# Optimization experiments

Hardware: AMD Instinct MI355X
Metric: run time of the kernel (lower is better)

## Reference

```python
import jax, jax.numpy as jnp
import numpy as np

B, S, D = 4, 2048, 1024
H = 16
HD = D // H  # head_dim = key_dim = value_dim = 64


def setup_inputs() -> dict:
    key = jax.random.key(0)
    ks = jax.random.split(key, 4)
    scale = (2.0 / (D + D)) ** 0.5  # xavier_normal for square weight
    return {
        "hidden_states": jax.random.normal(ks[0], (B, S, D), dtype=jnp.float32),
        "Wq": jax.random.normal(ks[1], (D, D), dtype=jnp.float32) * scale,
        "bq": jnp.zeros((D,), dtype=jnp.float32),
        "Wk": jax.random.normal(ks[2], (D, D), dtype=jnp.float32) * scale,
        "bk": jnp.zeros((D,), dtype=jnp.float32),
        "Wv": jax.random.normal(ks[3], (D, D), dtype=jnp.float32) * scale,
        "bv": jnp.zeros((D,), dtype=jnp.float32),
    }


def _split_heads(x):
    # [B, S, H*HD] -> [B, H, S, HD]
    b, s, _ = x.shape
    return x.reshape(b, s, H, HD).transpose(0, 2, 1, 3)


def reference(hidden_states, Wq, bq, Wk, bk, Wv, bv):
    # Linear projections (torch Linear: x @ W.T + b)
    q = _split_heads(hidden_states @ Wq.T + bq)  # [B,H,S,HD]
    k = _split_heads(hidden_states @ Wk.T + bk)
    v = _split_heads(hidden_states @ Wv.T + bv)
    scores = jnp.einsum("bhqd,bhkd->bhqk", q, k) / jnp.sqrt(jnp.float32(HD))
    probs = jax.nn.softmax(scores, axis=-1)
    out = jnp.einsum("bhqk,bhkd->bhqd", probs, v)  # [B,H,S,HD]
    # merge heads -> [B, S, H*HD]
    return out.transpose(0, 2, 1, 3).reshape(B, S, H * HD)
```

## Files before the change

### kernel.cpp

```cpp
#include <hip/hip_runtime.h>
#include <math.h>

#define SB 4
#define SS 2048
#define SD 1024
#define SH 16
#define SHD 64
#define SM (SB * SS)

using f32x4 = __attribute__((ext_vector_type(4))) float;
using h8    = __attribute__((ext_vector_type(8))) _Float16;
using h4    = __attribute__((ext_vector_type(4))) _Float16;
using fp16x2 = __fp16 __attribute__((ext_vector_type(2)));
using fp16x4 = __fp16 __attribute__((ext_vector_type(4)));
using u32x4 = __attribute__((ext_vector_type(4))) unsigned int;

__device__ __forceinline__ unsigned short f2h(float x) {
  _Float16 h = (_Float16)x;
  return __builtin_bit_cast(unsigned short, h);
}

__device__ __forceinline__ void gld_lds16(const unsigned short* g, unsigned short* l) {
  __builtin_amdgcn_global_load_lds(
      (const __attribute__((address_space(1))) unsigned int*)g,
      (__attribute__((address_space(3))) unsigned int*)l, 16, 0, 0);
}

__global__ __launch_bounds__(256) void cvt4h(const float* __restrict__ in,
                                             unsigned short* __restrict__ out, int n4) {
  int i = blockIdx.x * 256 + threadIdx.x;
  if (i >= n4) return;
  float4 v = ((const float4*)in)[i];
  unsigned long long r = (unsigned long long)f2h(v.x)
                       | ((unsigned long long)f2h(v.y) << 16)
                       | ((unsigned long long)f2h(v.z) << 32)
                       | ((unsigned long long)f2h(v.w) << 48);
  ((unsigned long long*)out)[i] = r;
}

__global__ __launch_bounds__(256) void cvt3w(const float* __restrict__ w0, const float* __restrict__ w1,
                                             const float* __restrict__ w2,
                                             unsigned short* __restrict__ o0, unsigned short* __restrict__ o1,
                                             unsigned short* __restrict__ o2) {
  const int z = blockIdx.y;
  const float* in = (z == 0) ? w0 : (z == 1) ? w1 : w2;
  unsigned short* out = (z == 0) ? o0 : (z == 1) ? o1 : o2;
  int i = blockIdx.x * 256 + threadIdx.x;
  float4 v = ((const float4*)in)[i];
  unsigned long long r = (unsigned long long)f2h(v.x)
                       | ((unsigned long long)f2h(v.y) << 16)
                       | ((unsigned long long)f2h(v.z) << 32)
                       | ((unsigned long long)f2h(v.w) << 48);
  ((unsigned long long*)out)[i] = r;
}

__global__ __launch_bounds__(256) void gemm_qkv(
    const unsigned short* __restrict__ Xh,
    const unsigned short* __restrict__ Wqh, const unsigned short* __restrict__ Wkh,
    const unsigned short* __restrict__ Wvh,
    const float* __restrict__ bq, const float* __restrict__ bk, const float* __restrict__ bv,
    unsigned short* __restrict__ Qh, unsigned short* __restrict__ Kh,
    unsigned short* __restrict__ Vt) {
  __shared__ unsigned short lA[128 * 64];
  __shared__ unsigned short lB[128 * 64];
  const int L = blockIdx.x;
  const int xcd = L & 7, rr = L >> 3;
  const int mloc = rr & 7, widx = rr >> 3;
  const int tNi = widx & 7, z = widx >> 3;
  const int tM = (xcd * 8 + mloc) * 128, tN = tNi * 128;

  const unsigned short* W = (z == 0) ? Wqh : (z == 1) ? Wkh : Wvh;
  const float* bias = (z == 0) ? bq : (z == 1) ? bk : bv;

  const int tid = threadIdx.x;
  const int wave = tid >> 6, lane = tid & 63;
  const int quad = lane >> 4, l16 = lane & 15;
  const int wr = (wave >> 1) * 64, wc = (wave & 1) * 64;

  f32x4 acc[4][4] = {};

  const int rB = tid >> 3;
  const int colOff = (((tid & 7) ^ (rB & 7))) * 8;
  const unsigned short* gA[4];
  const unsigned short* gB[4];
#pragma unroll
  for (int i = 0; i < 4; ++i) {
    gA[i] = Xh + (size_t)(tM + i * 32 + rB) * SD + colOff;
    gB[i] = W  + (size_t)(tN + i * 32 + rB) * SD + colOff;
  }
  unsigned short* dA[4];
  unsigned short* dB[4];
#pragma unroll
  for (int i = 0; i < 4; ++i) {
    dA[i] = lA + (i * 256 + wave * 64) * 8;
    dB[i] = lB + (i * 256 + wave * 64) * 8;
  }
  const int swl = l16 & 7;

  if (z == 2) {
    for (int k0 = 0; k0 < SD; k0 += 64) {
      __syncthreads();
#pragma unroll
      for (int i = 0; i < 4; ++i) gld_lds16(gA[i] + k0, dA[i]);
#pragma unroll
      for (int i = 0; i < 4; ++i) gld_lds16(gB[i] + k0, dB[i]);
      __syncthreads();
#pragma unroll
      for (int ks = 0; ks < 2; ++ks) {
        h8 af[4], bf[4];
#pragma unroll
        for (int mi = 0; mi < 4; ++mi)
          af[mi] = *(const h8*)(lA + (wr + mi * 16 + l16) * 64 + (((ks * 4 + quad) ^ swl) * 8));
#pragma unroll
        for (int ni = 0; ni < 4; ++ni)
          bf[ni] = *(const h8*)(lB + (wc + ni * 16 + l16) * 64 + (((ks * 4 + quad) ^ swl) * 8));
#pragma unroll
        for (int mi = 0; mi < 4; ++mi)
#pragma unroll
          for (int ni = 0; ni < 4; ++ni)
            acc[mi][ni] = __builtin_amdgcn_mfma_f32_16x16x32_f16(af[mi], bf[ni], acc[mi][ni], 0, 0, 0);
      }
    }
#pragma unroll
    for (int ni = 0; ni < 4; ++ni) {
      const int gn = tN + wc + ni * 16 + l16;
      const float bb = bias[gn];
#pragma unroll
      for (int mi = 0; mi < 4; ++mi) {
        const int gm = tM + wr + mi * 16 + quad * 4;
        const int vb = gm >> 11, vs = gm & 2047;
        unsigned long long wv = 0;
#pragma unroll
        for (int r = 0; r < 4; ++r)
          wv |= (unsigned long long)f2h(acc[mi][ni][r] + bb) << (16 * r);
        *(unsigned long long*)(Vt + (size_t)(vb * 1024 + gn) * SS + vs) = wv;
      }
    }
  } else {
    for (int k0 = 0; k0 < SD; k0 += 64) {
      __syncthreads();
#pragma unroll
      for (int i = 0; i < 4; ++i) gld_lds16(gA[i] + k0, dA[i]);
#pragma unroll
      for (int i = 0; i < 4; ++i) gld_lds16(gB[i] + k0, dB[i]);
      __syncthreads();
#pragma unroll
      for (int ks = 0; ks < 2; ++ks) {
        h8 af[4], bf[4];
#pragma unroll
        for (int mi = 0; mi < 4; ++mi)
          af[mi] = *(const h8*)(lA + (wr + mi * 16 + l16) * 64 + (((ks * 4 + quad) ^ swl) * 8));
#pragma unroll
        for (int ni = 0; ni < 4; ++ni)
          bf[ni] = *(const h8*)(lB + (wc + ni * 16 + l16) * 64 + (((ks * 4 + quad) ^ swl) * 8));
#pragma unroll
        for (int mi = 0; mi < 4; ++mi)
#pragma unroll
          for (int ni = 0; ni < 4; ++ni)
            acc[mi][ni] = __builtin_amdgcn_mfma_f32_16x16x32_f16(bf[ni], af[mi], acc[mi][ni], 0, 0, 0);
      }
    }
    const float sc = (z == 0) ? 0.18033688011112042f : 1.0f;
    unsigned short* C = (z == 0) ? Qh : Kh;
#pragma unroll
    for (int mi = 0; mi < 4; ++mi) {
      const int gm = tM + wr + mi * 16 + l16;
#pragma unroll
      for (int ni = 0; ni < 4; ++ni) {
        const int gnb = tN + wc + ni * 16 + quad * 4;
        const float4 bb4 = *(const float4*)(bias + gnb);
        unsigned long long wv;
        wv  = (unsigned long long)f2h((acc[mi][ni][0] + bb4.x) * sc);
        wv |= (unsigned long long)f2h((acc[mi][ni][1] + bb4.y) * sc) << 16;
        wv |= (unsigned long long)f2h((acc[mi][ni][2] + bb4.z) * sc) << 32;
        wv |= (unsigned long long)f2h((acc[mi][ni][3] + bb4.w) * sc) << 48;
        *(unsigned long long*)(C + (size_t)gm * SD + gnb) = wv;
      }
    }
  }
}

__global__ __launch_bounds__(256, 4) void attn(const unsigned short* __restrict__ Qh,
                                               const unsigned short* __restrict__ Kh,
                                               const unsigned short* __restrict__ Vt,
                                               float* __restrict__ out) {
  __shared__ unsigned short lK[2][64 * 64];
  __shared__ unsigned short lV[2][64 * 64];
  const int tid = threadIdx.x;
  const int wave = tid >> 6, lane = tid & 63;
  const int quad = lane >> 4, l16 = lane & 15;
  const int bid = blockIdx.x;
  const int bh = bid & 63, qt = bid >> 6;
  const int b = bh >> 4, h = bh & 15;
  const int qs = qt * 128 + wave * 16;

  const unsigned short* qp0 = Qh + ((size_t)(b * SS + qs + l16)) * SD + h * 64 + quad * 8;
  h8 aq[2][2];
#pragma unroll
  for (int x = 0; x < 2; ++x) {
    aq[x][0] = *(const h8*)(qp0 + (size_t)(x * 64) * SD);
    aq[x][1] = *(const h8*)(qp0 + (size_t)(x * 64) * SD + 32);
  }

  const int row0 = tid >> 3, cs0 = (tid & 7) ^ (row0 & 7);
  const int row1 = row0 + 32, cs1 = (tid & 7) ^ (row1 & 7);
  const unsigned short* kS0 = Kh + ((size_t)(b * SS + row0)) * SD + h * 64 + cs0 * 8;
  const unsigned short* kS1 = Kh + ((size_t)(b * SS + row1)) * SD + h * 64 + cs1 * 8;
  const unsigned short* vS0 = Vt + ((size_t)(bh * 64 + row0)) * SS + cs0 * 8;
  const unsigned short* vS1 = Vt + ((size_t)(bh * 64 + row1)) * SS + cs1 * 8;
  unsigned short* dK0 = &lK[0][wave * 512];
  unsigned short* dK1 = &lK[0][2048 + wave * 512];
  unsigned short* dV0 = &lV[0][wave * 512];
  unsigned short* dV1 = &lV[0][2048 + wave * 512];

  f32x4 ov[2][4] = {};
  float lacc[2] = {0.f, 0.f};
  const int swl = l16 & 7;
  const int ko0 = (quad ^ swl) * 8, ko1 = ((4 + quad) ^ swl) * 8;

  gld_lds16(kS0, dK0); gld_lds16(kS1, dK1);
  gld_lds16(vS0, dV0); gld_lds16(vS1, dV1);
  kS0 += 64 * SD; kS1 += 64 * SD; vS0 += 64; vS1 += 64;

  for (int kt = 0; kt < 32; ++kt) {
    const int buf = kt & 1;
    __syncthreads();
    if (kt < 31) {
      const int o = (buf ^ 1) * 64 * 64;
      gld_lds16(kS0, dK0 + o); gld_lds16(kS1, dK1 + o);
      gld_lds16(vS0, dV0 + o); gld_lds16(vS1, dV1 + o);
      kS0 += 64 * SD; kS1 += 64 * SD; vS0 += 64; vS1 += 64;
    }
    const unsigned short* Kt = lK[buf];
    const unsigned short* Vl = lV[buf];

    f32x4 s[2][4];
    __builtin_amdgcn_s_setprio(1);
#pragma unroll
    for (int nt = 0; nt < 4; ++nt) {
      const unsigned short* kr = Kt + (nt * 16 + l16) * 64;
      h8 kf0 = *(const h8*)(kr + ko0);
      h8 kf1 = *(const h8*)(kr + ko1);
#pragma unroll
      for (int x = 0; x < 2; ++x) {
        f32x4 z = {};
        z = __builtin_amdgcn_mfma_f32_16x16x32_f16(kf0, aq[x][0], z, 0, 0, 0);
        s[x][nt] = __builtin_amdgcn_mfma_f32_16x16x32_f16(kf1, aq[x][1], z, 0, 0, 0);
      }
    }
    __builtin_amdgcn_s_setprio(0);

    h8 pb[2][2];
#pragma unroll
    for (int x = 0; x < 2; ++x) {
      unsigned ul[4], uh[4];
      float la = 0.f;
#pragma unroll
      for (int g = 0; g < 4; ++g) {
        float p0 = __builtin_amdgcn_exp2f(s[x][g][0]);
        float p1 = __builtin_amdgcn_exp2f(s[x][g][1]);
        float p2 = __builtin_amdgcn_exp2f(s[x][g][2]);
        float p3 = __builtin_amdgcn_exp2f(s[x][g][3]);
        la += (p0 + p1) + (p2 + p3);
        ul[g] = __builtin_bit_cast(unsigned, __builtin_amdgcn_cvt_pkrtz(p0, p1));
        uh[g] = __builtin_bit_cast(unsigned, __builtin_amdgcn_cvt_pkrtz(p2, p3));
      }
      lacc[x] += la;
      auto sl0 = __builtin_amdgcn_permlane32_swap(ul[0], ul[1], false, false);
      auto tl0 = __builtin_amdgcn_permlane16_swap(sl0[0], sl0[1], false, false);
      auto sh0 = __builtin_amdgcn_permlane32_swap(uh[0], uh[1], false, false);
      auto th0 = __builtin_amdgcn_permlane16_swap(sh0[0], sh0[1], false, false);
      u32x4 w0 = {tl0[0], th0[0], tl0[1], th0[1]};
      pb[x][0] = __builtin_bit_cast(h8, w0);
      auto sl1 = __builtin_amdgcn_permlane32_swap(ul[2], ul[3], false, false);
      auto tl1 = __builtin_amdgcn_permlane16_swap(sl1[0], sl1[1], false, false);
      auto sh1 = __builtin_amdgcn_permlane32_swap(uh[2], uh[3], false, false);
      auto th1 = __builtin_amdgcn_permlane16_swap(sh1[0], sh1[1], false, false);
      u32x4 w1 = {tl1[0], th1[0], tl1[1], th1[1]};
      pb[x][1] = __builtin_bit_cast(h8, w1);
    }

    __builtin_amdgcn_s_setprio(1);
#pragma unroll
    for (int f = 0; f < 4; ++f) {
      const unsigned short* vr = Vl + (f * 16 + l16) * 64;
      h8 v0 = *(const h8*)(vr + ko0);
      h8 v1 = *(const h8*)(vr + ko1);
#pragma unroll
      for (int x = 0; x < 2; ++x) {
        ov[x][f] = __builtin_amdgcn_mfma_f32_16x16x32_f16(v0, pb[x][0], ov[x][f], 0, 0, 0);
        ov[x][f] = __builtin_amdgcn_mfma_f32_16x16x32_f16(v1, pb[x][1], ov[x][f], 0, 0, 0);
      }
    }
    __builtin_amdgcn_s_setprio(0);
  }

#pragma unroll
  for (int x = 0; x < 2; ++x) {
    float lt = lacc[x];
    lt += __shfl_xor(lt, 16);
    lt += __shfl_xor(lt, 32);
    const float inv = 1.0f / lt;
    float* orow = out + ((size_t)(b * SS + qs + x * 64 + l16)) * SD + h * 64 + quad * 4;
#pragma unroll
    for (int f = 0; f < 4; ++f) {
      float4 w;
      w.x = ov[x][f][0] * inv; w.y = ov[x][f][1] * inv;
      w.z = ov[x][f][2] * inv; w.w = ov[x][f][3] * inv;
      *(float4*)(orow + f * 16) = w;
    }
  }
}

extern "C" void kernel_launch(void* const* d_in, const int* in_sizes, int n_in,
                              void* d_out, int out_size, void* d_ws, size_t ws_size,
                              hipStream_t stream) {
  const float* hs = (const float*)d_in[0];
  const float* Wq = (const float*)d_in[1];
  const float* bq = (const float*)d_in[2];
  const float* Wk = (const float*)d_in[3];
  const float* bk = (const float*)d_in[4];
  const float* Wv = (const float*)d_in[5];
  const float* bv = (const float*)d_in[6];
  float* out = (float*)d_out;

  char* ws = (char*)d_ws;
  unsigned short* Xh  = (unsigned short*)(ws);
  unsigned short* Wqh = (unsigned short*)(ws + 16777216);
  unsigned short* Wkh = (unsigned short*)(ws + 16777216 + 2097152);
  unsigned short* Wvh = (unsigned short*)(ws + 16777216 + 2 * 2097152);
  unsigned short* Qh  = (unsigned short*)(ws + 16777216 + 3 * 2097152);
  unsigned short* Kh  = Qh + (size_t)SM * SD;
  unsigned short* Vt  = Kh + (size_t)SM * SD;

  cvt4h<<<dim3(8192), dim3(256), 0, stream>>>(hs, Xh, SM * SD / 4);
  cvt3w<<<dim3(1024, 3), dim3(256), 0, stream>>>(Wq, Wk, Wv, Wqh, Wkh, Wvh);
  gemm_qkv<<<dim3(1536), dim3(256), 0, stream>>>(
      Xh, Wqh, Wkh, Wvh, bq, bk, bv, Qh, Kh, Vt);
  attn<<<dim3(SB * SH * (SS / 128)), dim3(256), 0, stream>>>(Qh, Kh, Vt, out);
}
```

Measured before the change: 242.7 us.

## Merge conversion kernels and triple-buffer attention with 512-thread blocks

The two fp32-to-fp16 conversion kernels become a single launch. The attention kernel grows to 8 waves per block covering 256 query rows, so each K/V tile is loaded once and shared by twice as many queries, with each thread issuing one K and one V load. The double-buffered loop becomes a triple-buffered pipeline that waits with explicit vmcnt and a raw s_barrier, which lets loads run two tiles ahead. The trade-offs are more LDS per block, fewer blocks in the grid, and fragile hand-written waitcnt synchronisation.

```diff
diff --git a/kernel.cpp b/kernel.cpp
--- a/kernel.cpp
+++ b/kernel.cpp
@@ -26,32 +26,28 @@
       (__attribute__((address_space(3))) unsigned int*)l, 16, 0, 0);
 }
 
-__global__ __launch_bounds__(256) void cvt4h(const float* __restrict__ in,
-                                             unsigned short* __restrict__ out, int n4) {
-  int i = blockIdx.x * 256 + threadIdx.x;
-  if (i >= n4) return;
+__global__ __launch_bounds__(256) void cvt_all(const float* __restrict__ hs,
+    const float* __restrict__ w0, const float* __restrict__ w1, const float* __restrict__ w2,
+    unsigned short* __restrict__ xo, unsigned short* __restrict__ o0,
+    unsigned short* __restrict__ o1, unsigned short* __restrict__ o2) {
+  const int bid = blockIdx.x;
+  const float* in;
+  unsigned short* out;
+  int i;
+  if (bid < 8192) {
+    in = hs; out = xo; i = bid * 256 + threadIdx.x;
+  } else {
+    const int r = bid - 8192, z = r >> 10;
+    in = (z == 0) ? w0 : (z == 1) ? w1 : w2;
+    out = (z == 0) ? o0 : (z == 1) ? o1 : o2;
+    i = (r & 1023) * 256 + threadIdx.x;
+  }
   float4 v = ((const float4*)in)[i];
-  unsigned long long r = (unsigned long long)f2h(v.x)
-                       | ((unsigned long long)f2h(v.y) << 16)
-                       | ((unsigned long long)f2h(v.z) << 32)
-                       | ((unsigned long long)f2h(v.w) << 48);
-  ((unsigned long long*)out)[i] = r;
-}
-
-__global__ __launch_bounds__(256) void cvt3w(const float* __restrict__ w0, const float* __restrict__ w1,
-                                             const float* __restrict__ w2,
-                                             unsigned short* __restrict__ o0, unsigned short* __restrict__ o1,
-                                             unsigned short* __restrict__ o2) {
-  const int z = blockIdx.y;
-  const float* in = (z == 0) ? w0 : (z == 1) ? w1 : w2;
-  unsigned short* out = (z == 0) ? o0 : (z == 1) ? o1 : o2;
-  int i = blockIdx.x * 256 + threadIdx.x;
-  float4 v = ((const float4*)in)[i];
-  unsigned long long r = (unsigned long long)f2h(v.x)
-                       | ((unsigned long long)f2h(v.y) << 16)
-                       | ((unsigned long long)f2h(v.z) << 32)
-                       | ((unsigned long long)f2h(v.w) << 48);
-  ((unsigned long long*)out)[i] = r;
+  unsigned long long rr = (unsigned long long)f2h(v.x)
+                        | ((unsigned long long)f2h(v.y) << 16)
+                        | ((unsigned long long)f2h(v.z) << 32)
+                        | ((unsigned long long)f2h(v.w) << 48);
+  ((unsigned long long*)out)[i] = rr;
 }
 
 __global__ __launch_bounds__(256) void gemm_qkv(
@@ -180,120 +176,132 @@
   }
 }
 
-__global__ __launch_bounds__(256, 4) void attn(const unsigned short* __restrict__ Qh,
+__global__ __launch_bounds__(512, 4) void attn(const unsigned short* __restrict__ Qh,
                                                const unsigned short* __restrict__ Kh,
                                                const unsigned short* __restrict__ Vt,
                                                float* __restrict__ out) {
-  __shared__ unsigned short lK[2][64 * 64];
-  __shared__ unsigned short lV[2][64 * 64];
+  __shared__ unsigned short lK[3][64 * 64];
+  __shared__ unsigned short lV[3][64 * 64];
   const int tid = threadIdx.x;
   const int wave = tid >> 6, lane = tid & 63;
   const int quad = lane >> 4, l16 = lane & 15;
   const int bid = blockIdx.x;
   const int bh = bid & 63, qt = bid >> 6;
   const int b = bh >> 4, h = bh & 15;
-  const int qs = qt * 128 + wave * 16;
+  const int qs = qt * 256 + wave * 16;
 
   const unsigned short* qp0 = Qh + ((size_t)(b * SS + qs + l16)) * SD + h * 64 + quad * 8;
   h8 aq[2][2];
 #pragma unroll
   for (int x = 0; x < 2; ++x) {
-    aq[x][0] = *(const h8*)(qp0 + (size_t)(x * 64) * SD);
-    aq[x][1] = *(const h8*)(qp0 + (size_t)(x * 64) * SD + 32);
+    aq[x][0] = *(const h8*)(qp0 + (size_t)(x * 128) * SD);
+    aq[x][1] = *(const h8*)(qp0 + (size_t)(x * 128) * SD + 32);
   }
 
   const int row0 = tid >> 3, cs0 = (tid & 7) ^ (row0 & 7);
-  const int row1 = row0 + 32, cs1 = (tid & 7) ^ (row1 & 7);
   const unsigned short* kS0 = Kh + ((size_t)(b * SS + row0)) * SD + h * 64 + cs0 * 8;
-  const unsigned short* kS1 = Kh + ((size_t)(b * SS + row1)) * SD + h * 64 + cs1 * 8;
   const unsigned short* vS0 = Vt + ((size_t)(bh * 64 + row0)) * SS + cs0 * 8;
-  const unsigned short* vS1 = Vt + ((size_t)(bh * 64 + row1)) * SS + cs1 * 8;
   unsigned short* dK0 = &lK[0][wave * 512];
-  unsigned short* dK1 = &lK[0][2048 + wave * 512];
   unsigned short* dV0 = &lV[0][wave * 512];
-  unsigned short* dV1 = &lV[0][2048 + wave * 512];
 
   f32x4 ov[2][4] = {};
   float lacc[2] = {0.f, 0.f};
   const int swl = l16 & 7;
   const int ko0 = (quad ^ swl) * 8, ko1 = ((4 + quad) ^ swl) * 8;
 
-  gld_lds16(kS0, dK0); gld_lds16(kS1, dK1);
-  gld_lds16(vS0, dV0); gld_lds16(vS1, dV1);
-  kS0 += 64 * SD; kS1 += 64 * SD; vS0 += 64; vS1 += 64;
-
-  for (int kt = 0; kt < 32; ++kt) {
-    const int buf = kt & 1;
-    __syncthreads();
-    if (kt < 31) {
-      const int o = (buf ^ 1) * 64 * 64;
-      gld_lds16(kS0, dK0 + o); gld_lds16(kS1, dK1 + o);
-      gld_lds16(vS0, dV0 + o); gld_lds16(vS1, dV1 + o);
-      kS0 += 64 * SD; kS1 += 64 * SD; vS0 += 64; vS1 += 64;
-    }
-    const unsigned short* Kt = lK[buf];
-    const unsigned short* Vl = lV[buf];
-
-    f32x4 s[2][4];
-    __builtin_amdgcn_s_setprio(1);
-#pragma unroll
-    for (int nt = 0; nt < 4; ++nt) {
-      const unsigned short* kr = Kt + (nt * 16 + l16) * 64;
-      h8 kf0 = *(const h8*)(kr + ko0);
-      h8 kf1 = *(const h8*)(kr + ko1);
-#pragma unroll
-      for (int x = 0; x < 2; ++x) {
-        f32x4 z = {};
-        z = __builtin_amdgcn_mfma_f32_16x16x32_f16(kf0, aq[x][0], z, 0, 0, 0);
-        s[x][nt] = __builtin_amdgcn_mfma_f32_16x16x32_f16(kf1, aq[x][1], z, 0, 0, 0);
-      }
-    }
-    __builtin_amdgcn_s_setprio(0);
-
-    h8 pb[2][2];
-#pragma unroll
-    for (int x = 0; x < 2; ++x) {
-      unsigned ul[4], uh[4];
-      float la = 0.f;
-#pragma unroll
-      for (int g = 0; g < 4; ++g) {
-        float p0 = __builtin_amdgcn_exp2f(s[x][g][0]);
-        float p1 = __builtin_amdgcn_exp2f(s[x][g][1]);
-        float p2 = __builtin_amdgcn_exp2f(s[x][g][2]);
-        float p3 = __builtin_amdgcn_exp2f(s[x][g][3]);
-        la += (p0 + p1) + (p2 + p3);
-        ul[g] = __builtin_bit_cast(unsigned, __builtin_amdgcn_cvt_pkrtz(p0, p1));
-        uh[g] = __builtin_bit_cast(unsigned, __builtin_amdgcn_cvt_pkrtz(p2, p3));
-      }
-      lacc[x] += la;
-      auto sl0 = __builtin_amdgcn_permlane32_swap(ul[0], ul[1], false, false);
-      auto tl0 = __builtin_amdgcn_permlane16_swap(sl0[0], sl0[1], false, false);
-      auto sh0 = __builtin_amdgcn_permlane32_swap(uh[0], uh[1], false, false);
-      auto th0 = __builtin_amdgcn_permlane16_swap(sh0[0], sh0[1], false, false);
-      u32x4 w0 = {tl0[0], th0[0], tl0[1], th0[1]};
-      pb[x][0] = __builtin_bit_cast(h8, w0);
-      auto sl1 = __builtin_amdgcn_permlane32_swap(ul[2], ul[3], false, false);
-      auto tl1 = __builtin_amdgcn_permlane16_swap(sl1[0], sl1[1], false, false);
-      auto sh1 = __builtin_amdgcn_permlane32_swap(uh[2], uh[3], false, false);
-      auto th1 = __builtin_amdgcn_permlane16_swap(sh1[0], sh1[1], false, false);
-      u32x4 w1 = {tl1[0], th1[0], tl1[1], th1[1]};
-      pb[x][1] = __builtin_bit_cast(h8, w1);
-    }
-
-    __builtin_amdgcn_s_setprio(1);
-#pragma unroll
-    for (int f = 0; f < 4; ++f) {
-      const unsigned short* vr = Vl + (f * 16 + l16) * 64;
-      h8 v0 = *(const h8*)(vr + ko0);
-      h8 v1 = *(const h8*)(vr + ko1);
-#pragma unroll
-      for (int x = 0; x < 2; ++x) {
-        ov[x][f] = __builtin_amdgcn_mfma_f32_16x16x32_f16(v0, pb[x][0], ov[x][f], 0, 0, 0);
-        ov[x][f] = __builtin_amdgcn_mfma_f32_16x16x32_f16(v1, pb[x][1], ov[x][f], 0, 0, 0);
-      }
-    }
-    __builtin_amdgcn_s_setprio(0);
-  }
+#define STAGE(BUF) do { \
+    gld_lds16(kS0, dK0 + (BUF) * 4096); \
+    gld_lds16(vS0, dV0 + (BUF) * 4096); \
+    kS0 += 64 * SD; vS0 += 64; \
+  } while (0)
+
+#define COMPUTE(BUF) do { \
+    const unsigned short* Kt = lK[BUF]; \
+    const unsigned short* Vl = lV[BUF]; \
+    f32x4 s[2][4]; \
+    __builtin_amdgcn_s_setprio(1); \
+    _Pragma("unroll") \
+    for (int nt = 0; nt < 4; ++nt) { \
+      const unsigned short* kr = Kt + (nt * 16 + l16) * 64; \
+      h8 kf0 = *(const h8*)(kr + ko0); \
+      h8 kf1 = *(const h8*)(kr + ko1); \
+      _Pragma("unroll") \
+      for (int x = 0; x < 2; ++x) { \
+        f32x4 z = {}; \
+        z = __builtin_amdgcn_mfma_f32_16x16x32_f16(kf0, aq[x][0], z, 0, 0, 0); \
+        s[x][nt] = __builtin_amdgcn_mfma_f32_16x16x32_f16(kf1, aq[x][1], z, 0, 0, 0); \
+      } \
+    } \
+    __builtin_amdgcn_s_setprio(0); \
+    h8 pb[2][2]; \
+    _Pragma("unroll") \
+    for (int x = 0; x < 2; ++x) { \
+      unsigned ul[4], uh[4]; \
+      float la = 0.f; \
+      _Pragma("unroll") \
+      for (int g = 0; g < 4; ++g) { \
+        float p0 = __builtin_amdgcn_exp2f(s[x][g][0]); \
+        float p1 = __builtin_amdgcn_exp2f(s[x][g][1]); \
+        float p2 = __builtin_amdgcn_exp2f(s[x][g][2]); \
+        float p3 = __builtin_amdgcn_exp2f(s[x][g][3]); \
+        la += (p0 + p1) + (p2 + p3); \
+        ul[g] = __builtin_bit_cast(unsigned, __builtin_amdgcn_cvt_pkrtz(p0, p1)); \
+        uh[g] = __builtin_bit_cast(unsigned, __builtin_amdgcn_cvt_pkrtz(p2, p3)); \
+      } \
+      lacc[x] += la; \
+      auto sl0 = __builtin_amdgcn_permlane32_swap(ul[0], ul[1], false, false); \
+      auto tl0 = __builtin_amdgcn_permlane16_swap(sl0[0], sl0[1], false, false); \
+      auto sh0 = __builtin_amdgcn_permlane32_swap(uh[0], uh[1], false, false); \
+      auto th0 = __builtin_amdgcn_permlane16_swap(sh0[0], sh0[1], false, false); \
+      u32x4 w0 = {tl0[0], th0[0], tl0[1], th0[1]}; \
+      pb[x][0] = __builtin_bit_cast(h8, w0); \
+      auto sl1 = __builtin_amdgcn_permlane32_swap(ul[2], ul[3], false, false); \
+      auto tl1 = __builtin_amdgcn_permlane16_swap(sl1[0], sl1[1], false, false); \
+      auto sh1 = __builtin_amdgcn_permlane32_swap(uh[2], uh[3], false, false); \
+      auto th1 = __builtin_amdgcn_permlane16_swap(sh1[0], sh1[1], false, false); \
+      u32x4 w1 = {tl1[0], th1[0], tl1[1], th1[1]}; \
+      pb[x][1] = __builtin_bit_cast(h8, w1); \
+    } \
+    __builtin_amdgcn_s_setprio(1); \
+    _Pragma("unroll") \
+    for (int f = 0; f < 4; ++f) { \
+      const unsigned short* vr = Vl + (f * 16 + l16) * 64; \
+      h8 v0 = *(const h8*)(vr + ko0); \
+      h8 v1 = *(const h8*)(vr + ko1); \
+      _Pragma("unroll") \
+      for (int x = 0; x < 2; ++x) { \
+        ov[x][f] = __builtin_amdgcn_mfma_f32_16x16x32_f16(v0, pb[x][0], ov[x][f], 0, 0, 0); \
+        ov[x][f] = __builtin_amdgcn_mfma_f32_16x16x32_f16(v1, pb[x][1], ov[x][f], 0, 0, 0); \
+      } \
+    } \
+    __builtin_amdgcn_s_setprio(0); \
+  } while (0)
+
+#define PHASE(BUF, PBUF) do { \
+    asm volatile("s_waitcnt vmcnt(2)" ::: "memory"); \
+    __builtin_amdgcn_s_barrier(); \
+    STAGE(PBUF); \
+    COMPUTE(BUF); \
+  } while (0)
+
+  STAGE(0);
+  STAGE(1);
+
+  for (int j = 0; j < 10; ++j) {
+    PHASE(0, 2);
+    PHASE(1, 0);
+    PHASE(2, 1);
+  }
+  asm volatile("s_waitcnt vmcnt(2)" ::: "memory");
+  __builtin_amdgcn_s_barrier();
+  COMPUTE(0);
+  asm volatile("s_waitcnt vmcnt(0)" ::: "memory");
+  __builtin_amdgcn_s_barrier();
+  COMPUTE(1);
+
+#undef PHASE
+#undef COMPUTE
+#undef STAGE
 
 #pragma unroll
   for (int x = 0; x < 2; ++x) {
@@ -301,7 +309,7 @@
     lt += __shfl_xor(lt, 16);
     lt += __shfl_xor(lt, 32);
     const float inv = 1.0f / lt;
-    float* orow = out + ((size_t)(b * SS + qs + x * 64 + l16)) * SD + h * 64 + quad * 4;
+    float* orow = out + ((size_t)(b * SS + qs + x * 128 + l16)) * SD + h * 64 + quad * 4;
 #pragma unroll
     for (int f = 0; f < 4; ++f) {
       float4 w;
@@ -333,9 +341,8 @@
   unsigned short* Kh  = Qh + (size_t)SM * SD;
   unsigned short* Vt  = Kh + (size_t)SM * SD;
 
-  cvt4h<<<dim3(8192), dim3(256), 0, stream>>>(hs, Xh, SM * SD / 4);
-  cvt3w<<<dim3(1024, 3), dim3(256), 0, stream>>>(Wq, Wk, Wv, Wqh, Wkh, Wvh);
+  cvt_all<<<dim3(8192 + 3072), dim3(256), 0, stream>>>(hs, Wq, Wk, Wv, Xh, Wqh, Wkh, Wvh);
   gemm_qkv<<<dim3(1536), dim3(256), 0, stream>>>(
       Xh, Wqh, Wkh, Wvh, bq, bk, bv, Qh, Kh, Vt);
-  attn<<<dim3(SB * SH * (SS / 128)), dim3(256), 0, stream>>>(Qh, Kh, Vt, out);
-}
+  attn<<<dim3(SB * SH * (SS / 256)), dim3(512), 0, stream>>>(Qh, Kh, Vt, out);
+}
```

After: 568.4 us. +134.2%, slower.

## Permute V-transpose store layout to drop permlane shuffles; merge conversion kernels

Applied to the files above, without the earlier changes.

The QKV GEMM epilogue now writes the transposed V with a permuted sequence order inside each 32-row group. This ordering matches the register layout of the packed softmax probabilities in attention, so the permlane32/permlane16 swap sequence that previously rearranged P before the PV MFMA is removed. Separately, the activation and weight fp16 conversion kernels are fused into one launch to save a kernel launch. Correctness depends on the store permutation exactly matching the lane layout the swaps used to produce.

```diff
diff --git a/kernel.cpp b/kernel.cpp
--- a/kernel.cpp
+++ b/kernel.cpp
@@ -10,9 +10,7 @@
 
 using f32x4 = __attribute__((ext_vector_type(4))) float;
 using h8    = __attribute__((ext_vector_type(8))) _Float16;
-using h4    = __attribute__((ext_vector_type(4))) _Float16;
 using fp16x2 = __fp16 __attribute__((ext_vector_type(2)));
-using fp16x4 = __fp16 __attribute__((ext_vector_type(4)));
 using u32x4 = __attribute__((ext_vector_type(4))) unsigned int;
 
 __device__ __forceinline__ unsigned short f2h(float x) {
@@ -26,32 +24,28 @@
       (__attribute__((address_space(3))) unsigned int*)l, 16, 0, 0);
 }
 
-__global__ __launch_bounds__(256) void cvt4h(const float* __restrict__ in,
-                                             unsigned short* __restrict__ out, int n4) {
-  int i = blockIdx.x * 256 + threadIdx.x;
-  if (i >= n4) return;
+__global__ __launch_bounds__(256) void cvt_all(const float* __restrict__ hs,
+    const float* __restrict__ w0, const float* __restrict__ w1, const float* __restrict__ w2,
+    unsigned short* __restrict__ xo, unsigned short* __restrict__ o0,
+    unsigned short* __restrict__ o1, unsigned short* __restrict__ o2) {
+  const int bid = blockIdx.x;
+  const float* in;
+  unsigned short* out;
+  int i;
+  if (bid < 8192) {
+    in = hs; out = xo; i = bid * 256 + threadIdx.x;
+  } else {
+    const int r = bid - 8192, z = r >> 10;
+    in = (z == 0) ? w0 : (z == 1) ? w1 : w2;
+    out = (z == 0) ? o0 : (z == 1) ? o1 : o2;
+    i = (r & 1023) * 256 + threadIdx.x;
+  }
   float4 v = ((const float4*)in)[i];
-  unsigned long long r = (unsigned long long)f2h(v.x)
-                       | ((unsigned long long)f2h(v.y) << 16)
-                       | ((unsigned long long)f2h(v.z) << 32)
-                       | ((unsigned long long)f2h(v.w) << 48);
-  ((unsigned long long*)out)[i] = r;
-}
-
-__global__ __launch_bounds__(256) void cvt3w(const float* __restrict__ w0, const float* __restrict__ w1,
-                                             const float* __restrict__ w2,
-                                             unsigned short* __restrict__ o0, unsigned short* __restrict__ o1,
-                                             unsigned short* __restrict__ o2) {
-  const int z = blockIdx.y;
-  const float* in = (z == 0) ? w0 : (z == 1) ? w1 : w2;
-  unsigned short* out = (z == 0) ? o0 : (z == 1) ? o1 : o2;
-  int i = blockIdx.x * 256 + threadIdx.x;
-  float4 v = ((const float4*)in)[i];
-  unsigned long long r = (unsigned long long)f2h(v.x)
-                       | ((unsigned long long)f2h(v.y) << 16)
-                       | ((unsigned long long)f2h(v.z) << 32)
-                       | ((unsigned long long)f2h(v.w) << 48);
-  ((unsigned long long*)out)[i] = r;
+  unsigned long long rr = (unsigned long long)f2h(v.x)
+                        | ((unsigned long long)f2h(v.y) << 16)
+                        | ((unsigned long long)f2h(v.z) << 32)
+                        | ((unsigned long long)f2h(v.w) << 48);
+  ((unsigned long long*)out)[i] = rr;
 }
 
 __global__ __launch_bounds__(256) void gemm_qkv(
@@ -127,8 +121,9 @@
       const float bb = bias[gn];
 #pragma unroll
       for (int mi = 0; mi < 4; ++mi) {
-        const int gm = tM + wr + mi * 16 + quad * 4;
-        const int vb = gm >> 11, vs = gm & 2047;
+        const int gmb = tM + wr + mi * 16;
+        const int sp = (gmb & ~31) + quad * 8 + (mi & 1) * 4;
+        const int vb = gmb >> 11, vs = sp & 2047;
         unsigned long long wv = 0;
 #pragma unroll
         for (int r = 0; r < 4; ++r)
@@ -266,17 +261,9 @@
         uh[g] = __builtin_bit_cast(unsigned, __builtin_amdgcn_cvt_pkrtz(p2, p3));
       }
       lacc[x] += la;
-      auto sl0 = __builtin_amdgcn_permlane32_swap(ul[0], ul[1], false, false);
-      auto tl0 = __builtin_amdgcn_permlane16_swap(sl0[0], sl0[1], false, false);
-      auto sh0 = __builtin_amdgcn_permlane32_swap(uh[0], uh[1], false, false);
-      auto th0 = __builtin_amdgcn_permlane16_swap(sh0[0], sh0[1], false, false);
-      u32x4 w0 = {tl0[0], th0[0], tl0[1], th0[1]};
+      u32x4 w0 = {ul[0], uh[0], ul[1], uh[1]};
       pb[x][0] = __builtin_bit_cast(h8, w0);
-      auto sl1 = __builtin_amdgcn_permlane32_swap(ul[2], ul[3], false, false);
-      auto tl1 = __builtin_amdgcn_permlane16_swap(sl1[0], sl1[1], false, false);
-      auto sh1 = __builtin_amdgcn_permlane32_swap(uh[2], uh[3], false, false);
-      auto th1 = __builtin_amdgcn_permlane16_swap(sh1[0], sh1[1], false, false);
-      u32x4 w1 = {tl1[0], th1[0], tl1[1], th1[1]};
+      u32x4 w1 = {ul[2], uh[2], ul[3], uh[3]};
       pb[x][1] = __builtin_bit_cast(h8, w1);
     }
 
@@ -333,8 +320,7 @@
   unsigned short* Kh  = Qh + (size_t)SM * SD;
   unsigned short* Vt  = Kh + (size_t)SM * SD;
 
-  cvt4h<<<dim3(8192), dim3(256), 0, stream>>>(hs, Xh, SM * SD / 4);
-  cvt3w<<<dim3(1024, 3), dim3(256), 0, stream>>>(Wq, Wk, Wv, Wqh, Wkh, Wvh);
+  cvt_all<<<dim3(8192 + 3072), dim3(256), 0, stream>>>(hs, Wq, Wk, Wv, Xh, Wqh, Wkh, Wvh);
   gemm_qkv<<<dim3(1536), dim3(256), 0, stream>>>(
       Xh, Wqh, Wkh, Wvh, bq, bk, bv, Qh, Kh, Vt);
   attn<<<dim3(SB * SH * (SS / 128)), dim3(256), 0, stream>>>(Qh, Kh, Vt, out);
```

New measurement: 230.6 us. -4.9%, faster.
